# Optimization experiments

Measured on AMD Instinct MI355X. Metric: run time of the kernel, lower is better.

Reference implementation:

```python
import jax, jax.numpy as jnp
import numpy as np

WIN, SIGMA = 11, 1.5
C1, C2, EPS = 0.01 ** 2, 0.03 ** 2, 1e-8


def _gauss_window(win=WIN, sigma=SIGMA):
    coords = jnp.arange(win, dtype=jnp.float32) - (win - 1) / 2
    g = jnp.exp(-coords ** 2 / (2 * sigma ** 2))
    g = g / g.sum()
    return (g[:, None] * g[None, :])[None, None, :, :]


def setup_inputs() -> dict:
    key = jax.random.key(0)
    k1, k2 = jax.random.split(key)
    N, C, H, W = 32, 1, 512, 512
    x = jax.random.uniform(k1, (N, C, H, W), dtype=jnp.float32)
    y = jax.random.uniform(k2, (N, C, H, W), dtype=jnp.float32)
    w = _gauss_window()
    return {"x": x, "y": y, "w": w}


def _conv(x, w):
    pad = w.shape[-1] // 2
    return jax.lax.conv_general_dilated(
        x, w, window_strides=(1, 1), padding=[(pad, pad), (pad, pad)],
        dimension_numbers=("NCHW", "OIHW", "NCHW"))


def reference(x, y, w):
    w = w.astype(x.dtype)
    n = x.shape[0]
    # One fused conv over all five planes stacked on the batch dim.
    stacked = jnp.concatenate([x, y, x * x, y * y, x * y], axis=0)
    conv = _conv(stacked, w)
    mu_x, mu_y, ex2, ey2, exy = (conv[i * n:(i + 1) * n] for i in range(5))
    mu_x2, mu_y2, mu_xy = mu_x ** 2, mu_y ** 2, mu_x * mu_y
    sig_x2 = ex2 - mu_x2
    sig_y2 = ey2 - mu_y2
    sig_xy = exy - mu_xy
    num = (2 * mu_xy + C1) * (2 * sig_xy + C2)
    den = (mu_x2 + mu_y2 + C1) * (sig_x2 + sig_y2 + C2)
    return jnp.clip(num / (den + EPS), 0.0, 1.0).mean()
```

## Files before the change

kernel.cpp:

```cpp
#include <hip/hip_runtime.h>


typedef float v2f __attribute__((ext_vector_type(2)));
typedef float v4f __attribute__((ext_vector_type(4)));

#define IMG_H 512
#define IMG_W 512
#define NIMG  32
#define NT    256
#define RROWS 22
#define ITERS (RROWS + 10)
#define CH    11
#define NCHNK 3
#define LDSW  524

#define C1F  1.0e-4f
#define C2F  9.0e-4f
#define EPSF 1.0e-8f

static __device__ __forceinline__ v2f pkfma(float s, v2f a, v2f b) {
    v2f sv = {s, s};
    return __builtin_elementwise_fma(sv, a, b);
}

__global__ __launch_bounds__(NT) void ssim_kernel(
    const float* __restrict__ xg, const float* __restrict__ yg,
    const float* __restrict__ wg, float* __restrict__ out)
{
    const int t    = threadIdx.x;
    const int lane = t & 63;
    const int chnk = blockIdx.x;
    const int img  = blockIdx.y;
    const int r0   = chnk * RROWS;
    const int c0   = 2 * t;

    const float* xb = xg + (size_t)img * (IMG_H * IMG_W);
    const float* yb = yg + (size_t)img * (IMG_H * IMG_W);

    __shared__ alignas(16) v2f ssd[CH][LDSW];
    __shared__ float wredS[4];

    float rs = 0.f;
    if (lane < 11) {
        #pragma unroll
        for (int j = 0; j < 11; ++j) rs += wg[lane * 11 + j];
    }
    float g[11];
    #pragma unroll
    for (int k = 0; k < 11; ++k) {
        int gi = __shfl(__float_as_int(rs), k, 64);
        g[k] = __int_as_float(__builtin_amdgcn_readfirstlane(gi));
    }

    const v2f z2 = {0.f, 0.f};

    if (t < 55)               { ssd[t / 5][1 + t % 5] = z2; }
    if (t >= 128 && t < 183)  { const int u = t - 128; ssd[u / 5][518 + u % 5] = z2; }

    v2f px[CH], py[CH];
    #pragma unroll
    for (int m = 0; m < CH; ++m) {
        const int r = r0 - 5 + m;
        if ((unsigned)r < IMG_H) {
            px[m] = *(const v2f*)(xb + (size_t)r * IMG_W + c0);
            py[m] = *(const v2f*)(yb + (size_t)r * IMG_W + c0);
        } else { px[m] = z2; py[m] = z2; }
    }

    v2f rSD[CH][2], rQ[CH][2];

    float acc = 0.f;

    #pragma unroll 1
    for (int c = 0; c < NCHNK; ++c) {
        #pragma unroll
        for (int m = 0; m < CH; ++m) {
            const v2f sv = px[m] + py[m];
            const v2f dv = px[m] - py[m];
            v4f st = {sv.x, dv.x, sv.y, dv.y};
            *(v4f*)&ssd[m][6 + c0] = st;
        }
        __syncthreads();

        if (c < NCHNK - 1) {
            #pragma unroll
            for (int m = 0; m < CH; ++m) {
                const int r = r0 + 6 + CH * c + m;
                if ((unsigned)r < IMG_H) {
                    px[m] = *(const v2f*)(xb + (size_t)r * IMG_W + c0);
                    py[m] = *(const v2f*)(yb + (size_t)r * IMG_W + c0);
                } else { px[m] = z2; py[m] = z2; }
            }
        }

        #pragma unroll
        for (int s = 0; s < CH; ++s) {
            const int i = CH * c + s;
            v2f hA = z2, hB = z2, qA = z2, qB = z2;
            #pragma unroll
            for (int m = 0; m < 7; ++m) {
                const v4f w4 = *(const v4f*)&ssd[s][c0 + 2 * m];
                const v2f e0 = {w4.x, w4.y};
                const v2f e1 = {w4.z, w4.w};
                {
                    const int j = 2 * m;
                    if (j >= 1) {
                        const v2f f0 = e0 * e0;
                        if (j <= 11) {
                            hA = pkfma(g[j - 1], e0, hA);
                            qA = pkfma(g[j - 1], f0, qA);
                        }
                        if (j >= 2) {
                            hB = pkfma(g[j - 2], e0, hB);
                            qB = pkfma(g[j - 2], f0, qB);
                        }
                    }
                }
                {
                    const int j = 2 * m + 1;
                    if (j <= 12) {
                        const v2f f1 = e1 * e1;
                        if (j <= 11) {
                            hA = pkfma(g[j - 1], e1, hA);
                            qA = pkfma(g[j - 1], f1, qA);
                        }
                        if (j >= 2) {
                            hB = pkfma(g[j - 2], e1, hB);
                            qB = pkfma(g[j - 2], f1, qB);
                        }
                    }
                }
            }
            rSD[s][0] = hA; rSD[s][1] = hB;
            rQ[s][0]  = qA; rQ[s][1]  = qB;

            if (i >= 10 && i < ITERS) {
                const int orow = r0 + i - 10;
                if (orow < IMG_H) {
                    #pragma unroll
                    for (int cc = 0; cc < 2; ++cc) {
                        v2f mSD = z2, mQ = z2;
                        #pragma unroll
                        for (int j = 0; j < 11; ++j) {
                            const int sl = (s + 1 + j) % 11;
                            mSD = pkfma(g[j], rSD[sl][cc], mSD);
                            mQ  = pkfma(g[j], rQ[sl][cc],  mQ);
                        }
                        const v2f t2 = mSD * mSD;
                        const float a    = 0.5f  * (t2.x + t2.y);
                        const float muxy = 0.25f * (t2.x - t2.y);
                        const float ep   = 0.5f  * (mQ.x + mQ.y);
                        const float eq   = 0.25f * (mQ.x - mQ.y);
                        const float sxy  = eq - muxy;
                        const float ssum = ep - a;
                        const float num  = fmaf(2.f, muxy, C1F) * fmaf(2.f, sxy, C2F);
                        const float den  = (a + C1F) * (ssum + C2F);
                        float v = num * __builtin_amdgcn_rcpf(den + EPSF);
                        acc += fminf(fmaxf(v, 0.f), 1.f);
                    }
                }
            }
        }
        __syncthreads();
    }

    #pragma unroll
    for (int off = 32; off > 0; off >>= 1)
        acc += __shfl_down(acc, off, 64);
    if (lane == 0) wredS[t >> 6] = acc;
    __syncthreads();
    if (t == 0) {
        const float tot = (wredS[0] + wredS[1]) + (wredS[2] + wredS[3]);
        atomicAdd(out, tot * (1.0f / (float)((size_t)NIMG * IMG_H * IMG_W)));
    }
}

extern "C" void kernel_launch(void* const* d_in, const int* in_sizes, int n_in,
                              void* d_out, int out_size, void* d_ws, size_t ws_size,
                              hipStream_t stream) {
    const float* x = (const float*)d_in[0];
    const float* y = (const float*)d_in[1];
    const float* w = (const float*)d_in[2];
    float* out = (float*)d_out;

    hipMemsetAsync(out, 0, sizeof(float), stream);

    dim3 grid((IMG_H + RROWS - 1) / RROWS, NIMG);
    ssim_kernel<<<grid, dim3(NT), 0, stream>>>(x, y, w, out);
}
```

Measured before the change: 117.8 us.

## Give each wave a private LDS segment with halo and stream rows without barriers

Each wavefront now owns a 128-column strip and stages one row at a time into its own small LDS segment. Edge lanes load the 6-column halo, so no block-wide __syncthreads is needed and only one row of x/y sits in registers instead of eleven. Rows per block go from 22 to 23, which changes the grid size. The trade-offs are extra redundant halo loads, lane divergence on the halo path, and only a single-row prefetch distance, which may expose global-memory latency.

```diff
diff --git a/kernel.cpp b/kernel.cpp
--- a/kernel.cpp
+++ b/kernel.cpp
@@ -8,11 +8,9 @@
 #define IMG_W 512
 #define NIMG  32
 #define NT    256
-#define RROWS 22
+#define RROWS 23
 #define ITERS (RROWS + 10)
-#define CH    11
-#define NCHNK 3
-#define LDSW  524
+#define SEGW  144
 
 #define C1F  1.0e-4f
 #define C2F  9.0e-4f
@@ -29,15 +27,18 @@
 {
     const int t    = threadIdx.x;
     const int lane = t & 63;
+    const int wv   = t >> 6;
     const int chnk = blockIdx.x;
     const int img  = blockIdx.y;
     const int r0   = chnk * RROWS;
-    const int c0   = 2 * t;
+    const int C0   = 128 * wv;
+    const int cown = C0 + 2 * lane;
+    const int c0l  = 2 * lane;
 
     const float* xb = xg + (size_t)img * (IMG_H * IMG_W);
     const float* yb = yg + (size_t)img * (IMG_H * IMG_W);
 
-    __shared__ alignas(16) v2f ssd[CH][LDSW];
+    __shared__ alignas(16) v2f seg[4][SEGW];
     __shared__ float wredS[4];
 
     float rs = 0.f;
@@ -54,52 +55,69 @@
 
     const v2f z2 = {0.f, 0.f};
 
-    if (t < 55)               { ssd[t / 5][1 + t % 5] = z2; }
-    if (t >= 128 && t < 183)  { const int u = t - 128; ssd[u / 5][518 + u % 5] = z2; }
-
-    v2f px[CH], py[CH];
-    #pragma unroll
-    for (int m = 0; m < CH; ++m) {
-        const int r = r0 - 5 + m;
+    const bool isH = (lane < 3) || (lane >= 61);
+    const int  hcol = (lane < 3) ? (C0 - 6 + 2 * lane)
+                                 : (C0 + 128 + 2 * (lane - 61));
+    const int  hidx = (lane < 3) ? (2 * lane) : (134 + 2 * (lane - 61));
+
+    v2f px, py, hx, hy;
+    {
+        const int r = r0 - 5;
+        px = z2; py = z2; hx = z2; hy = z2;
         if ((unsigned)r < IMG_H) {
-            px[m] = *(const v2f*)(xb + (size_t)r * IMG_W + c0);
-            py[m] = *(const v2f*)(yb + (size_t)r * IMG_W + c0);
-        } else { px[m] = z2; py[m] = z2; }
-    }
-
-    v2f rSD[CH][2], rQ[CH][2];
+            const float* xr = xb + (size_t)r * IMG_W;
+            const float* yr = yb + (size_t)r * IMG_W;
+            px = *(const v2f*)(xr + cown);
+            py = *(const v2f*)(yr + cown);
+            if (isH && (unsigned)hcol < IMG_W) {
+                hx = *(const v2f*)(xr + hcol);
+                hy = *(const v2f*)(yr + hcol);
+            }
+        }
+    }
+
+    v2f rSD[11][2], rQ[11][2];
 
     float acc = 0.f;
 
     #pragma unroll 1
-    for (int c = 0; c < NCHNK; ++c) {
+    for (int base = 0; base < ITERS; base += 11) {
         #pragma unroll
-        for (int m = 0; m < CH; ++m) {
-            const v2f sv = px[m] + py[m];
-            const v2f dv = px[m] - py[m];
-            v4f st = {sv.x, dv.x, sv.y, dv.y};
-            *(v4f*)&ssd[m][6 + c0] = st;
-        }
-        __syncthreads();
-
-        if (c < NCHNK - 1) {
-            #pragma unroll
-            for (int m = 0; m < CH; ++m) {
-                const int r = r0 + 6 + CH * c + m;
+        for (int s = 0; s < 11; ++s) {
+            const int i = base + s;
+
+            {
+                const v2f sv = px + py;
+                const v2f dv = px - py;
+                v4f st = {sv.x, dv.x, sv.y, dv.y};
+                *(v4f*)&seg[wv][6 + c0l] = st;
+                if (isH) {
+                    const v2f hs = hx + hy;
+                    const v2f hd = hx - hy;
+                    v4f ht = {hs.x, hd.x, hs.y, hd.y};
+                    *(v4f*)&seg[wv][hidx] = ht;
+                }
+            }
+
+            if (i < ITERS - 1) {
+                const int r = r0 - 4 + i;
+                px = z2; py = z2; hx = z2; hy = z2;
                 if ((unsigned)r < IMG_H) {
-                    px[m] = *(const v2f*)(xb + (size_t)r * IMG_W + c0);
-                    py[m] = *(const v2f*)(yb + (size_t)r * IMG_W + c0);
-                } else { px[m] = z2; py[m] = z2; }
-            }
-        }
-
-        #pragma unroll
-        for (int s = 0; s < CH; ++s) {
-            const int i = CH * c + s;
+                    const float* xr = xb + (size_t)r * IMG_W;
+                    const float* yr = yb + (size_t)r * IMG_W;
+                    px = *(const v2f*)(xr + cown);
+                    py = *(const v2f*)(yr + cown);
+                    if (isH && (unsigned)hcol < IMG_W) {
+                        hx = *(const v2f*)(xr + hcol);
+                        hy = *(const v2f*)(yr + hcol);
+                    }
+                }
+            }
+
             v2f hA = z2, hB = z2, qA = z2, qB = z2;
             #pragma unroll
             for (int m = 0; m < 7; ++m) {
-                const v4f w4 = *(const v4f*)&ssd[s][c0 + 2 * m];
+                const v4f w4 = *(const v4f*)&seg[wv][c0l + 2 * m];
                 const v2f e0 = {w4.x, w4.y};
                 const v2f e1 = {w4.z, w4.w};
                 {
@@ -134,7 +152,7 @@
             rSD[s][0] = hA; rSD[s][1] = hB;
             rQ[s][0]  = qA; rQ[s][1]  = qB;
 
-            if (i >= 10 && i < ITERS) {
+            if (i >= 10) {
                 const int orow = r0 + i - 10;
                 if (orow < IMG_H) {
                     #pragma unroll
@@ -161,13 +179,12 @@
                 }
             }
         }
-        __syncthreads();
     }
 
     #pragma unroll
     for (int off = 32; off > 0; off >>= 1)
         acc += __shfl_down(acc, off, 64);
-    if (lane == 0) wredS[t >> 6] = acc;
+    if (lane == 0) wredS[wv] = acc;
     __syncthreads();
     if (t == 0) {
         const float tot = (wredS[0] + wredS[1]) + (wredS[2] + wredS[3]);
```

After: 117.2 us. No clear change (-0.5%).
